# Kernel tuning notes

Hardware: AMD Instinct MI355X
Metric: run time of the kernel (lower is better)

The kernel has to match this reference:

```python
import jax, jax.numpy as jnp
import numpy as np

N = 50000          # nodes
E = 1600000        # edges (avg degree 32)
G = 16             # graphs in batch
H = 128            # hidden_dim
HOP = 3
IN_DIM = 1


def setup_inputs() -> dict:
    key = jax.random.key(0)
    ks = jax.random.split(key, 12)
    s = 1.0 / np.sqrt(H)
    return {
        "x": jax.random.normal(ks[0], (N, IN_DIM), jnp.float32),
        "edge_index": jax.random.randint(ks[1], (2, E), 0, N, jnp.int64),
        "edge_attr": jax.random.uniform(ks[2], (E, 1), jnp.float32),
        "batch": jnp.sort(jax.random.randint(ks[3], (N,), 0, G, jnp.int64)),
        "W1": jax.random.normal(ks[4], (HOP, H, IN_DIM), jnp.float32) * s,
        "W2": jax.random.normal(ks[5], (HOP, H, H), jnp.float32) * s,
        "W3": jax.random.normal(ks[6], (HOP, H, H), jnp.float32) * s,
        "W4": jax.random.normal(ks[7], (HOP, H, 1), jnp.float32) * s,
        "W5": jax.random.normal(ks[8], (1, 2 * H), jnp.float32) * s,
        "b5": jnp.zeros((1,), jnp.float32),
        "W6": jax.random.normal(ks[9], (H, H), jnp.float32) * s,
        "W7": jax.random.normal(ks[10], (H, H), jnp.float32) * s,
    }


def reference(x, edge_index, edge_attr, batch, W1, W2, W3, W4, W5, b5, W6, W7):
    row, col = edge_index[0], edge_index[1]
    node_emb = jnp.zeros((N, H), x.dtype)
    for l in range(HOP):
        nfe = x @ W1[l].T                                        # [N,H]
        # gather neighbor embeddings along col, scatter-add to row
        ne_aggr = jax.ops.segment_sum(node_emb[col], row, num_segments=N)
        efe = jax.nn.relu(edge_attr @ W4[l].T)                   # [E,H]
        ee_aggr = jax.ops.segment_sum(efe, row, num_segments=N)  # [N,H]
        node_emb = jax.nn.relu(nfe + ne_aggr @ W2[l].T + ee_aggr @ W3[l].T)
    pooled = jax.ops.segment_sum(node_emb, batch, num_segments=G)  # [G,H]
    sum_emb = pooled @ W6.T                                        # [G,H]
    cat = jax.nn.relu(jnp.concatenate([sum_emb[batch], node_emb @ W7.T], axis=-1))
    return cat @ W5.T + b5                                         # [N,1]
```

## Files before the change

### kernel.cpp

```cpp
#include <hip/hip_runtime.h>
#include <hip/hip_bf16.h>

#define N_NODES 50000
#define N_EDGES 1600000
#define NGRAPH  16
#define HID     128

#define RPB   128
#define NB    ((N_NODES + RPB - 1) / RPB)
#define NBLK  256
#define EPB   ((N_EDGES + NBLK - 1) / NBLK)
#define P4CAP 6144

typedef unsigned int uint32;
typedef unsigned short ushort;
typedef unsigned char uchar;
typedef __attribute__((ext_vector_type(8))) short bf16x8;
typedef __attribute__((ext_vector_type(4))) float f32x4;
typedef __attribute__((ext_vector_type(2))) float f32x2;

__device__ __forceinline__ uint32 bf16r(float f) {
    uint32 b = __float_as_uint(f);
    return (b + 0x7fffu + ((b >> 16) & 1u)) >> 16;
}
__device__ __forceinline__ uint32 pack_bf16(float lo, float hi) {
    return bf16r(lo) | (bf16r(hi) << 16);
}

__global__ __launch_bounds__(256) void k_init(float* __restrict__ zp, int nz,
                                              const float* __restrict__ W2,
                                              const float* __restrict__ W7,
                                              const float* __restrict__ W3,
                                              const float* __restrict__ W4,
                                              ushort* __restrict__ wpack,
                                              float* __restrict__ v3) {
    int idx = blockIdx.x * 256 + threadIdx.x;
    if (idx < nz) zp[idx] = 0.f;
    if (idx < 4 * 16384) {
        int m = idx >> 14, f = idx & 16383;
        int j = f & 7, lane = (f >> 3) & 63, kk = (f >> 9) & 3, t = (f >> 11) & 7;
        int hp = t * 16 + (lane & 15);
        int k  = kk * 32 + ((lane >> 4) & 3) * 8 + j;
        const float* src = (m < 3) ? (W2 + m * HID * HID) : W7;
        wpack[idx] = (ushort)bf16r(src[hp * HID + k]);
    }
    if (idx < 3 * HID) {
        int l = idx / HID, hp = idx % HID;
        float acc = 0.f;
        for (int h = 0; h < HID; h++)
            acc += W3[l * HID * HID + hp * HID + h] * fmaxf(W4[l * HID + h], 0.f);
        v3[idx] = acc;
    }
}

__global__ __launch_bounds__(1024) void k_p1_hist(const int* __restrict__ row,
                                                  int* __restrict__ blkhist) {
    __shared__ int hist[NB];
    int tid = threadIdx.x, blk = blockIdx.x;
    for (int i = tid; i < NB; i += 1024) hist[i] = 0;
    __syncthreads();
    int s = blk * EPB, e = s + EPB; if (e > N_EDGES) e = N_EDGES;
    for (int i = s + tid; i < e; i += 1024)
        atomicAdd(&hist[row[i] >> 7], 1);
    __syncthreads();
    for (int i = tid; i < NB; i += 1024)
        blkhist[i * NBLK + blk] = hist[i];
}

__global__ __launch_bounds__(NBLK) void k_p2a(int* __restrict__ blkhist,
                                              int* __restrict__ btot) {
    __shared__ int sums[NBLK];
    int t = threadIdx.x, b = blockIdx.x;
    int v = blkhist[b * NBLK + t];
    sums[t] = v;
    __syncthreads();
    for (int d = 1; d < NBLK; d <<= 1) {
        int u = (t >= d) ? sums[t - d] : 0;
        __syncthreads();
        sums[t] += u;
        __syncthreads();
    }
    blkhist[b * NBLK + t] = sums[t] - v;
    if (t == NBLK - 1) btot[b] = sums[t];
}

__global__ __launch_bounds__(1024) void k_p3_part(const int* __restrict__ row,
                                                  const int* __restrict__ col,
                                                  const float* __restrict__ ea,
                                                  const int* __restrict__ blkhist,
                                                  const int* __restrict__ btot,
                                                  int2* __restrict__ pea) {
    __shared__ int sc[512];
    __shared__ int cur[NB];
    int tid = threadIdx.x, blk = blockIdx.x;
    if (tid < 512) sc[tid] = (tid < NB) ? btot[tid] : 0;
    __syncthreads();
    for (int d = 1; d < 512; d <<= 1) {
        int v = 0;
        if (tid < 512 && tid >= d) v = sc[tid - d];
        __syncthreads();
        if (tid < 512) sc[tid] += v;
        __syncthreads();
    }
    for (int i = tid; i < NB; i += 1024)
        cur[i] = (sc[i] - btot[i]) + blkhist[i * NBLK + blk];
    __syncthreads();
    int s = blk * EPB, e = s + EPB; if (e > N_EDGES) e = N_EDGES;
    for (int i = s + tid; i < e; i += 1024) {
        int r = row[i], c = col[i];
        float a = ea[i];
        int slot = atomicAdd(&cur[r >> 7], 1);
        pea[slot] = make_int2(((r & (RPB - 1)) << 16) | c, __float_as_int(a));
    }
}

__global__ __launch_bounds__(512) void k_p4(const int2* __restrict__ pea,
                                            const int* __restrict__ btot,
                                            const float* __restrict__ x,
                                            int* __restrict__ offs,
                                            float* __restrict__ ea_sum,
                                            int* __restrict__ csr,
                                            uchar* __restrict__ emb0,
                                            const float* __restrict__ w1l0,
                                            const float* __restrict__ v3l0) {
    __shared__ int2  cache[P4CAP];
    __shared__ int   red[512];
    __shared__ int   cnt[RPB];
    __shared__ float eas[RPB];
    __shared__ int   scan_s[RPB];
    __shared__ int   curp[RPB];
    int t = threadIdx.x, b = blockIdx.x;
    red[t] = (t < b) ? btot[t] : 0;
    __syncthreads();
    for (int d = 256; d > 0; d >>= 1) {
        if (t < d) red[t] += red[t + d];
        __syncthreads();
    }
    int s = red[0];
    int e = s + btot[b];
    int len = e - s;
    int clen = len < P4CAP ? len : P4CAP;
    for (int i = t; i < clen; i += 512) cache[i] = pea[s + i];
    if (t < RPB) { cnt[t] = 0; eas[t] = 0.f; }
    __syncthreads();
    for (int i = t; i < len; i += 512) {
        int2 p = (i < P4CAP) ? cache[i] : pea[s + i];
        int lr = ((uint32)p.x) >> 16;
        atomicAdd(&cnt[lr], 1);
        atomicAdd(&eas[lr], __int_as_float(p.y));
    }
    __syncthreads();
    if (t < RPB) scan_s[t] = cnt[t];
    __syncthreads();
    for (int d = 1; d < RPB; d <<= 1) {
        int v = 0;
        if (t < RPB && t >= d) v = scan_s[t - d];
        __syncthreads();
        if (t < RPB) scan_s[t] += v;
        __syncthreads();
    }
    int nbase = b * RPB;
    if (t < RPB) {
        int excl = scan_s[t] - cnt[t];
        int n = nbase + t;
        if (n < N_NODES) {
            offs[n] = s + excl;
            ea_sum[n] = eas[t];
        }
        curp[t] = s + excl;
    }
    if (b == NB - 1 && t == 0) offs[N_NODES] = e;
    __syncthreads();
    for (int i = t; i < len; i += 512) {
        int2 p = (i < P4CAP) ? cache[i] : pea[s + i];
        int slot = atomicAdd(&curp[((uint32)p.x) >> 16], 1);
        csr[slot] = p.x & 0xFFFF;
    }
    for (int i = t; i < RPB * 32; i += 512) {
        int lr = i >> 5, c4 = (i & 31) * 4;
        int n = nbase + lr;
        if (n < N_NODES) {
            float xv = x[n];
            float ev = eas[lr];
            float v0 = fmaxf(xv * w1l0[c4 + 0] + ev * v3l0[c4 + 0], 0.f) * 0.015625f;
            float v1 = fmaxf(xv * w1l0[c4 + 1] + ev * v3l0[c4 + 1], 0.f) * 0.015625f;
            float v2 = fmaxf(xv * w1l0[c4 + 2] + ev * v3l0[c4 + 2], 0.f) * 0.015625f;
            float v3v = fmaxf(xv * w1l0[c4 + 3] + ev * v3l0[c4 + 3], 0.f) * 0.015625f;
            int u = __builtin_amdgcn_cvt_pk_fp8_f32(v0, v1, 0, false);
            u = __builtin_amdgcn_cvt_pk_fp8_f32(v2, v3v, u, true);
            *(uint32*)(emb0 + (size_t)n * 128 + c4) = (uint32)u;
        }
    }
}

__global__ __launch_bounds__(256) void k_gather(const uchar* __restrict__ emb8,
                                                const int* __restrict__ offs,
                                                const int* __restrict__ csr,
                                                uint32* __restrict__ agg) {
    int node = (blockIdx.x * 256 + threadIdx.x) >> 6;
    int lane = threadIdx.x & 63;
    if (node >= N_NODES) return;
    int s = offs[node], e = offs[node + 1];
    float ax[8] = {0.f}, ay[8] = {0.f};
    for (int base = s; base < e; base += 64) {
        int idx = base + lane;
        int cv = (idx < e) ? csr[idx] : 0;
        int cnt = e - base; if (cnt > 64) cnt = 64;
        int j = 0;
        for (; j + 8 <= cnt; j += 8) {
            int h16[8];
#pragma unroll
            for (int u = 0; u < 8; u++) {
                int c = __shfl(cv, j + u);
                h16[u] = *(const ushort*)(emb8 + (size_t)c * 128 + 2 * lane);
            }
#pragma unroll
            for (int u = 0; u < 8; u++) {
                f32x2 d = __builtin_amdgcn_cvt_pk_f32_fp8(h16[u], false);
                ax[u] += d.x; ay[u] += d.y;
            }
        }
        for (; j < cnt; j++) {
            int c = __shfl(cv, j);
            int h = *(const ushort*)(emb8 + (size_t)c * 128 + 2 * lane);
            f32x2 d = __builtin_amdgcn_cvt_pk_f32_fp8(h, false);
            ax[0] += d.x; ay[0] += d.y;
        }
    }
    float rx = (((ax[0] + ax[1]) + (ax[2] + ax[3])) + ((ax[4] + ax[5]) + (ax[6] + ax[7]))) * 64.f;
    float ry = (((ay[0] + ay[1]) + (ay[2] + ay[3])) + ((ay[4] + ay[5]) + (ay[6] + ay[7]))) * 64.f;
    agg[(size_t)node * 64 + lane] = pack_bf16(rx, ry);
}

#define LROW 136

template <bool LAST>
__global__ __launch_bounds__(256) void k_gemm(const uint32* __restrict__ agg,
                                              const ushort* __restrict__ w2p,
                                              const float* __restrict__ w1l,
                                              const float* __restrict__ v3l,
                                              const float* __restrict__ x,
                                              const float* __restrict__ ea_sum,
                                              uchar* __restrict__ emb8Out,
                                              const ushort* __restrict__ w7p,
                                              const float* __restrict__ W5,
                                              float* __restrict__ outp,
                                              const int* __restrict__ batch,
                                              float* __restrict__ pooled) {
    __shared__ ushort tile[64 * LROW];
    __shared__ float redp[4][128];
    int tid = threadIdx.x;
    int tbase = blockIdx.x * 64;
    int wv = tid >> 6, lane = tid & 63;
    int n0 = lane & 15, quad = lane >> 4;
    int arow = wv * 16 + n0;
    bf16x8 a0 = {0,0,0,0,0,0,0,0}, a1 = a0, a2 = a0, a3 = a0;
    if (tbase + arow < N_NODES) {
        const bf16x8* ap = (const bf16x8*)(agg + (size_t)(tbase + arow) * 64);
        a0 = ap[0 + quad]; a1 = ap[4 + quad]; a2 = ap[8 + quad]; a3 = ap[12 + quad];
    }
    const bf16x8* wb = (const bf16x8*)w2p;
    f32x4 acc[8];
#pragma unroll
    for (int t = 0; t < 8; t++) {
        f32x4 c = {0.f, 0.f, 0.f, 0.f};
        c = __builtin_amdgcn_mfma_f32_16x16x32_bf16(a0, wb[(t * 4 + 0) * 64 + lane], c, 0, 0, 0);
        c = __builtin_amdgcn_mfma_f32_16x16x32_bf16(a1, wb[(t * 4 + 1) * 64 + lane], c, 0, 0, 0);
        c = __builtin_amdgcn_mfma_f32_16x16x32_bf16(a2, wb[(t * 4 + 2) * 64 + lane], c, 0, 0, 0);
        c = __builtin_amdgcn_mfma_f32_16x16x32_bf16(a3, wb[(t * 4 + 3) * 64 + lane], c, 0, 0, 0);
        acc[t] = c;
    }
    float xs[4], es[4];
#pragma unroll
    for (int r = 0; r < 4; r++) {
        int n = tbase + wv * 16 + quad * 4 + r;
        xs[r] = (n < N_NODES) ? x[n] : 0.f;
        es[r] = (n < N_NODES) ? ea_sum[n] : 0.f;
    }
    if (!LAST) {
        uchar* stile = (uchar*)tile;
#pragma unroll
        for (int t = 0; t < 8; t++) {
            int hp = t * 16 + n0;
            float w1v = w1l[hp], v3v = v3l[hp];
#pragma unroll
            for (int r = 0; r < 4; r++) {
                float v = fmaxf(acc[t][r] + xs[r] * w1v + es[r] * v3v, 0.f) * 0.015625f;
                int enc = __builtin_amdgcn_cvt_pk_fp8_f32(v, v, 0, false);
                stile[(wv * 16 + quad * 4 + r) * 136 + hp] = (uchar)(enc & 0xff);
            }
        }
        __syncthreads();
        int vn = N_NODES - tbase; if (vn > 64) vn = 64;
        for (int i = tid; i < 64 * 32; i += 256) {
            int r = i >> 5, c4 = (i & 31) * 4;
            if (r < vn) {
                uint32 u = *(const uint32*)&stile[r * 136 + c4];
                *(uint32*)(emb8Out + (size_t)(tbase + r) * 128 + c4) = u;
            }
        }
    } else {
        int nlast = tbase + 63; if (nlast > N_NODES - 1) nlast = N_NODES - 1;
        int g0 = batch[tbase];
        bool uni = (batch[nlast] == g0);
        int gr[4];
        if (!uni) {
#pragma unroll
            for (int r = 0; r < 4; r++) {
                int n = tbase + wv * 16 + quad * 4 + r;
                gr[r] = (n < N_NODES) ? batch[n] : 0;
            }
        }
        float st[8];
#pragma unroll
        for (int t = 0; t < 8; t++) {
            int hp = t * 16 + n0;
            float w1v = w1l[hp], v3v = v3l[hp];
            float stt = 0.f;
#pragma unroll
            for (int r = 0; r < 4; r++) {
                float v = fmaxf(acc[t][r] + xs[r] * w1v + es[r] * v3v, 0.f);
                tile[(wv * 16 + quad * 4 + r) * LROW + hp] = (ushort)bf16r(v);
                if (uni) {
                    stt += v;
                } else {
                    int n = tbase + wv * 16 + quad * 4 + r;
                    if (n < N_NODES) atomicAdd(&pooled[gr[r] * HID + hp], v);
                }
            }
            st[t] = stt;
        }
        if (uni) {
#pragma unroll
            for (int t = 0; t < 8; t++) {
                float v = st[t];
                v += __shfl_xor(v, 16);
                v += __shfl_xor(v, 32);
                if (lane < 16) redp[wv][t * 16 + lane] = v;
            }
        }
        __syncthreads();
        if (uni && tid < 128) {
            float sp = (redp[0][tid] + redp[1][tid]) + (redp[2][tid] + redp[3][tid]);
            atomicAdd(&pooled[g0 * HID + tid], sp);
        }
        bf16x8 b0 = *(const bf16x8*)&tile[arow * LROW + 0 * 32 + quad * 8];
        bf16x8 b1 = *(const bf16x8*)&tile[arow * LROW + 1 * 32 + quad * 8];
        bf16x8 b2 = *(const bf16x8*)&tile[arow * LROW + 2 * 32 + quad * 8];
        bf16x8 b3 = *(const bf16x8*)&tile[arow * LROW + 3 * 32 + quad * 8];
        const bf16x8* w7 = (const bf16x8*)w7p;
        float p[4] = {0.f, 0.f, 0.f, 0.f};
#pragma unroll
        for (int t = 0; t < 8; t++) {
            f32x4 c = {0.f, 0.f, 0.f, 0.f};
            c = __builtin_amdgcn_mfma_f32_16x16x32_bf16(b0, w7[(t * 4 + 0) * 64 + lane], c, 0, 0, 0);
            c = __builtin_amdgcn_mfma_f32_16x16x32_bf16(b1, w7[(t * 4 + 1) * 64 + lane], c, 0, 0, 0);
            c = __builtin_amdgcn_mfma_f32_16x16x32_bf16(b2, w7[(t * 4 + 2) * 64 + lane], c, 0, 0, 0);
            c = __builtin_amdgcn_mfma_f32_16x16x32_bf16(b3, w7[(t * 4 + 3) * 64 + lane], c, 0, 0, 0);
            float w5v = W5[128 + t * 16 + n0];
#pragma unroll
            for (int r = 0; r < 4; r++) p[r] += fmaxf(c[r], 0.f) * w5v;
        }
#pragma unroll
        for (int r = 0; r < 4; r++) {
            float v = p[r];
            v += __shfl_xor(v, 1);
            v += __shfl_xor(v, 2);
            v += __shfl_xor(v, 4);
            v += __shfl_xor(v, 8);
            int n = tbase + wv * 16 + quad * 4 + r;
            if (n0 == 0 && n < N_NODES) outp[n] = v;
        }
    }
}

__global__ __launch_bounds__(256) void k_tail(float* __restrict__ out,
                                              const int* __restrict__ batch,
                                              const float* __restrict__ pooled,
                                              const float* __restrict__ W6,
                                              const float* __restrict__ W5,
                                              const float* __restrict__ b5) {
    __shared__ float red[256];
    __shared__ int gsh[2];
    int t = threadIdx.x;
    int nbase = blockIdx.x * 256;
    int n = nbase + t;
    if (t == 0) gsh[0] = batch[nbase < N_NODES ? nbase : N_NODES - 1];
    if (t == 1) gsh[1] = batch[(nbase + 255) < N_NODES ? (nbase + 255) : N_NODES - 1];
    __syncthreads();
    int g_lo = gsh[0], g_hi = gsh[1];
    int hp = t & 127;
    int g = (t >> 7) ? g_hi : g_lo;
    const float* pg = pooled + g * HID;
    const float* wr = W6 + hp * HID;
    float acc = 0.f;
    for (int h = 0; h < HID; h++) acc += pg[h] * wr[h];
    red[t] = fmaxf(acc, 0.f) * W5[hp];
    __syncthreads();
    for (int d = 64; d > 0; d >>= 1) {
        if (hp < d) red[t] += red[t + d];
        __syncthreads();
    }
    float s_lo = red[0], s_hi = red[128];
    if (n < N_NODES) {
        int gn = batch[n];
        float s;
        if (gn == g_lo) s = s_lo;
        else if (gn == g_hi) s = s_hi;
        else {
            s = 0.f;
            const float* pg2 = pooled + gn * HID;
            for (int hp2 = 0; hp2 < HID; hp2++) {
                float a2 = 0.f;
                for (int h = 0; h < HID; h++) a2 += pg2[h] * W6[hp2 * HID + h];
                s += fmaxf(a2, 0.f) * W5[hp2];
            }
        }
        out[n] += s + b5[0];
    }
}

extern "C" void kernel_launch(void* const* d_in, const int* in_sizes, int n_in,
                              void* d_out, int out_size, void* d_ws, size_t ws_size,
                              hipStream_t stream) {
    (void)in_sizes; (void)n_in; (void)out_size; (void)ws_size;
    const float* x    = (const float*)d_in[0];
    const int*   ei   = (const int*)d_in[1];
    const float* ea   = (const float*)d_in[2];
    const int*   bat  = (const int*)d_in[3];
    const float* W1   = (const float*)d_in[4];
    const float* W2   = (const float*)d_in[5];
    const float* W3   = (const float*)d_in[6];
    const float* W4   = (const float*)d_in[7];
    const float* W5   = (const float*)d_in[8];
    const float* b5   = (const float*)d_in[9];
    const float* W6   = (const float*)d_in[10];
    const float* W7   = (const float*)d_in[11];
    float* out = (float*)d_out;

    const int* row = ei;
    const int* col = ei + N_EDGES;

    float* wsf = (float*)d_ws;
    int*   wsi = (int*)d_ws;
    size_t o = 0;
    float* pooled = wsf + o; o += NGRAPH * HID;
    size_t ztot = o;
    int*   offs   = wsi + o; o += N_NODES + 1;
    float* ea_sum = wsf + o; o += N_NODES;
    int*   btot   = wsi + o; o += NB;
    float* v3     = wsf + o; o += 3 * HID;
    int*   blkh   = wsi + o; o += NB * NBLK;
    o = (o + 3) & ~(size_t)3;
    ushort* wpack = (ushort*)(wsi + o); o += 4 * 16384 / 2;
    int*    csr   = wsi + o; o += N_EDGES;
    o = (o + 1) & ~(size_t)1;
    int2*   pea   = (int2*)(wsi + o); o += 2 * (size_t)N_EDGES;
    uint32* aggB  = (uint32*)(wsi + o); o += (size_t)N_NODES * 64;
    uchar*  emb8  = (uchar*)(wsi + o);  o += (size_t)N_NODES * 32;
    uchar*  emb0  = (uchar*)(wsi + o);  o += (size_t)N_NODES * 32;

    const ushort* w2p1 = wpack + 1 * 16384;
    const ushort* w2p2 = wpack + 2 * 16384;
    const ushort* w7p  = wpack + 3 * 16384;

    k_init<<<(4 * 16384 + 255) / 256, 256, 0, stream>>>(
        (float*)d_ws, (int)ztot, W2, W7, W3, W4, (ushort*)wpack, v3);
    k_p1_hist<<<NBLK, 1024, 0, stream>>>(row, blkh);
    k_p2a<<<NB, NBLK, 0, stream>>>(blkh, btot);
    k_p3_part<<<NBLK, 1024, 0, stream>>>(row, col, ea, blkh, btot, pea);
    k_p4<<<NB, 512, 0, stream>>>(pea, btot, x, offs, ea_sum, csr, emb0, W1, v3);
    k_gather<<<(N_NODES * 64 + 255) / 256, 256, 0, stream>>>(emb0, offs, csr, aggB);
    k_gemm<false><<<(N_NODES + 63) / 64, 256, 0, stream>>>(
        aggB, w2p1, W1 + 1 * HID, v3 + 1 * HID, x, ea_sum, emb8, nullptr, nullptr, nullptr,
        nullptr, nullptr);
    k_gather<<<(N_NODES * 64 + 255) / 256, 256, 0, stream>>>(emb8, offs, csr, aggB);
    k_gemm<true><<<(N_NODES + 63) / 64, 256, 0, stream>>>(
        aggB, w2p2, W1 + 2 * HID, v3 + 2 * HID, x, ea_sum, nullptr, w7p, W5, out, bat, pooled);
    k_tail<<<(N_NODES + 255) / 256, 256, 0, stream>>>(out, bat, pooled, W6, W5, b5);
}
```

Measured before the change: 267.6 us.

## Gather two nodes per wavefront with 4-byte fp8 loads per lane

The neighbor-aggregation kernel now maps two nodes to each 64-lane wavefront, with 32 lanes per node. Each lane loads 4 fp8 values (uint32) instead of 2, so each 128-byte row is fetched with wider loads and fewer wavefronts are needed. The two half-waves process their common edge count in full 32-wide chunks, then run a masked tail up to the longer node's length. The goal is fewer memory instructions per byte and less wave overhead, at the cost of lanes idling when paired nodes have uneven degrees.

```diff
diff --git a/kernel.cpp b/kernel.cpp
--- a/kernel.cpp
+++ b/kernel.cpp
@@ -193,43 +193,62 @@
     }
 }
 
-__global__ __launch_bounds__(256) void k_gather(const uchar* __restrict__ emb8,
+__global__ __launch_bounds__(256) void k_gather(const uchar* __restrict__ emb,
                                                 const int* __restrict__ offs,
                                                 const int* __restrict__ csr,
                                                 uint32* __restrict__ agg) {
-    int node = (blockIdx.x * 256 + threadIdx.x) >> 6;
+    int wv = threadIdx.x >> 6;
     int lane = threadIdx.x & 63;
-    if (node >= N_NODES) return;
-    int s = offs[node], e = offs[node + 1];
-    float ax[8] = {0.f}, ay[8] = {0.f};
-    for (int base = s; base < e; base += 64) {
-        int idx = base + lane;
+    int hl = lane & 31;
+    int node = blockIdx.x * 8 + wv * 2 + (lane >> 5);
+    bool valid = node < N_NODES;
+    int s = valid ? offs[node] : 0;
+    int e = valid ? offs[node + 1] : 0;
+    int len = e - s;
+    int olen = __shfl_xor(len, 32);
+    int clen = len < olen ? len : olen;
+    int mlen = len > olen ? len : olen;
+    f32x2 accLo[4], accHi[4];
+#pragma unroll
+    for (int i = 0; i < 4; i++) { accLo[i] = (f32x2){0.f, 0.f}; accHi[i] = (f32x2){0.f, 0.f}; }
+    int base = 0;
+    for (; base + 32 <= clen; base += 32) {
+        int cv = csr[s + base + hl];
+#pragma unroll
+        for (int j0 = 0; j0 < 32; j0 += 8) {
+            uint32 u[8];
+#pragma unroll
+            for (int q = 0; q < 8; q++) {
+                int c = __shfl(cv, j0 + q, 32);
+                u[q] = *(const uint32*)(emb + ((size_t)((uint32)c << 7) + (hl << 2)));
+            }
+#pragma unroll
+            for (int q = 0; q < 8; q++) {
+                accLo[q & 3] += __builtin_amdgcn_cvt_pk_f32_fp8((int)u[q], false);
+                accHi[q & 3] += __builtin_amdgcn_cvt_pk_f32_fp8((int)u[q], true);
+            }
+        }
+    }
+    for (; base < mlen; base += 32) {
+        int idx = s + base + hl;
         int cv = (idx < e) ? csr[idx] : 0;
-        int cnt = e - base; if (cnt > 64) cnt = 64;
-        int j = 0;
-        for (; j + 8 <= cnt; j += 8) {
-            int h16[8];
-#pragma unroll
-            for (int u = 0; u < 8; u++) {
-                int c = __shfl(cv, j + u);
-                h16[u] = *(const ushort*)(emb8 + (size_t)c * 128 + 2 * lane);
-            }
-#pragma unroll
-            for (int u = 0; u < 8; u++) {
-                f32x2 d = __builtin_amdgcn_cvt_pk_f32_fp8(h16[u], false);
-                ax[u] += d.x; ay[u] += d.y;
-            }
-        }
-        for (; j < cnt; j++) {
-            int c = __shfl(cv, j);
-            int h = *(const ushort*)(emb8 + (size_t)c * 128 + 2 * lane);
-            f32x2 d = __builtin_amdgcn_cvt_pk_f32_fp8(h, false);
-            ax[0] += d.x; ay[0] += d.y;
-        }
-    }
-    float rx = (((ax[0] + ax[1]) + (ax[2] + ax[3])) + ((ax[4] + ax[5]) + (ax[6] + ax[7]))) * 64.f;
-    float ry = (((ay[0] + ay[1]) + (ay[2] + ay[3])) + ((ay[4] + ay[5]) + (ay[6] + ay[7]))) * 64.f;
-    agg[(size_t)node * 64 + lane] = pack_bf16(rx, ry);
+        int rem = mlen - base; if (rem > 32) rem = 32;
+        for (int j = 0; j < rem; j++) {
+            int c = __shfl(cv, j, 32);
+            uint32 u = *(const uint32*)(emb + ((size_t)((uint32)c << 7) + (hl << 2)));
+            if (base + j >= len) u = 0;
+            accLo[j & 3] += __builtin_amdgcn_cvt_pk_f32_fp8((int)u, false);
+            accHi[j & 3] += __builtin_amdgcn_cvt_pk_f32_fp8((int)u, true);
+        }
+    }
+    f32x2 rl = (accLo[0] + accLo[1]) + (accLo[2] + accLo[3]);
+    f32x2 rh = (accHi[0] + accHi[1]) + (accHi[2] + accHi[3]);
+    if (valid) {
+        uint2 w;
+        w.x = pack_bf16(rl.x * 64.f, rl.y * 64.f);
+        w.y = pack_bf16(rh.x * 64.f, rh.y * 64.f);
+        *(uint2*)(agg + (size_t)node * 64 + hl * 2) = w;
+    }
 }
 
 #define LROW 136
@@ -470,11 +489,11 @@
     k_p2a<<<NB, NBLK, 0, stream>>>(blkh, btot);
     k_p3_part<<<NBLK, 1024, 0, stream>>>(row, col, ea, blkh, btot, pea);
     k_p4<<<NB, 512, 0, stream>>>(pea, btot, x, offs, ea_sum, csr, emb0, W1, v3);
-    k_gather<<<(N_NODES * 64 + 255) / 256, 256, 0, stream>>>(emb0, offs, csr, aggB);
+    k_gather<<<(N_NODES + 7) / 8, 256, 0, stream>>>(emb0, offs, csr, aggB);
     k_gemm<false><<<(N_NODES + 63) / 64, 256, 0, stream>>>(
         aggB, w2p1, W1 + 1 * HID, v3 + 1 * HID, x, ea_sum, emb8, nullptr, nullptr, nullptr,
         nullptr, nullptr);
-    k_gather<<<(N_NODES * 64 + 255) / 256, 256, 0, stream>>>(emb8, offs, csr, aggB);
+    k_gather<<<(N_NODES + 7) / 8, 256, 0, stream>>>(emb8, offs, csr, aggB);
     k_gemm<true><<<(N_NODES + 63) / 64, 256, 0, stream>>>(
         aggB, w2p2, W1 + 2 * HID, v3 + 2 * HID, x, ea_sum, nullptr, w7p, W5, out, bat, pooled);
     k_tail<<<(N_NODES + 255) / 256, 256, 0, stream>>>(out, bat, pooled, W6, W5, b5);
```

Measured after the change: 393.8 us. 1.47x slower.
